# Performance work log

Hardware: AMD Instinct MI355X
Metric: run time of the kernel (lower is better)

The kernel has to match this reference:

```python
import jax, jax.numpy as jnp
import numpy as np

COEF = 0.09          # amount of pixels flipped (salt + pepper)
SALT_VS_PEPPER = 0.5  # skimage default: half salt, half pepper


def setup_inputs() -> dict:
    key = jax.random.key(0)
    images = jax.random.uniform(key, (64, 3, 512, 512), dtype=jnp.float32)
    return {"images": images}


def reference(images):
    # Faithful to skimage.util.random_noise(image, mode='s&p', amount=COEF):
    #   flipped ~ U(0,1) <= amount selects corrupted pixels
    #   salted  ~ U(0,1) <= salt_vs_pepper splits them into salt (1.0) vs pepper (0.0)
    key = jax.random.key(42)
    k_flip, k_salt = jax.random.split(key)
    u_flip = jax.random.uniform(k_flip, images.shape, dtype=images.dtype)
    u_salt = jax.random.uniform(k_salt, images.shape, dtype=images.dtype)
    flipped = u_flip <= COEF
    salted = u_salt <= SALT_VS_PEPPER
    out = jnp.where(flipped & salted, jnp.asarray(1.0, images.dtype), images)
    out = jnp.where(flipped & ~salted, jnp.asarray(0.0, images.dtype), out)
    return out
```

## Files before the change

kernel.cpp:

```cpp
#include <hip/hip_runtime.h>
#include <stdint.h>


__host__ __device__ constexpr uint32_t rotl32(uint32_t x, int r) {
    return (x << r) | (x >> (32 - r));
}

struct TF2 { uint32_t a, b; };

__host__ __device__ constexpr TF2 threefry2x32(uint32_t k0, uint32_t k1,
                                               uint32_t x0, uint32_t x1) {
    const uint32_t ks0 = k0;
    const uint32_t ks1 = k1;
    const uint32_t ks2 = k0 ^ k1 ^ 0x1BD11BDAu;
    x0 += ks0; x1 += ks1;
    x0 += x1; x1 = rotl32(x1, 13); x1 ^= x0;
    x0 += x1; x1 = rotl32(x1, 15); x1 ^= x0;
    x0 += x1; x1 = rotl32(x1, 26); x1 ^= x0;
    x0 += x1; x1 = rotl32(x1,  6); x1 ^= x0;
    x0 += ks1; x1 += ks2 + 1u;
    x0 += x1; x1 = rotl32(x1, 17); x1 ^= x0;
    x0 += x1; x1 = rotl32(x1, 29); x1 ^= x0;
    x0 += x1; x1 = rotl32(x1, 16); x1 ^= x0;
    x0 += x1; x1 = rotl32(x1, 24); x1 ^= x0;
    x0 += ks2; x1 += ks0 + 2u;
    x0 += x1; x1 = rotl32(x1, 13); x1 ^= x0;
    x0 += x1; x1 = rotl32(x1, 15); x1 ^= x0;
    x0 += x1; x1 = rotl32(x1, 26); x1 ^= x0;
    x0 += x1; x1 = rotl32(x1,  6); x1 ^= x0;
    x0 += ks0; x1 += ks1 + 3u;
    x0 += x1; x1 = rotl32(x1, 17); x1 ^= x0;
    x0 += x1; x1 = rotl32(x1, 29); x1 ^= x0;
    x0 += x1; x1 = rotl32(x1, 16); x1 ^= x0;
    x0 += x1; x1 = rotl32(x1, 24); x1 ^= x0;
    x0 += ks1; x1 += ks2 + 4u;
    x0 += x1; x1 = rotl32(x1, 13); x1 ^= x0;
    x0 += x1; x1 = rotl32(x1, 15); x1 ^= x0;
    x0 += x1; x1 = rotl32(x1, 26); x1 ^= x0;
    x0 += x1; x1 = rotl32(x1,  6); x1 ^= x0;
    x0 += ks2; x1 += ks0 + 5u;
    return {x0, x1};
}

constexpr uint32_t SEED_HI = 0u;
constexpr uint32_t SEED_LO = 42u;
constexpr TF2 KFLIP = threefry2x32(SEED_HI, SEED_LO, 0u, 0u);
constexpr TF2 KSALT = threefry2x32(SEED_HI, SEED_LO, 0u, 1u);

constexpr uint32_t FLIP_T = (((uint32_t)((double)0.09f * 8388608.0)) + 1u) << 9;
constexpr uint32_t SALT_T = 0x80000200u;

__device__ __forceinline__ uint32_t rotl_d(uint32_t x, int r) {
    return __builtin_amdgcn_alignbit(x, x, 32u - (uint32_t)r);
}

#define TFR(rot) { x0 += x1; x1 = rotl_d(x1, rot); x1 ^= x0; }

template <uint32_t K0, uint32_t K1>
__device__ __forceinline__ uint32_t tf_bits(uint32_t ctr) {
    constexpr uint32_t K2 = K0 ^ K1 ^ 0x1BD11BDAu;
    uint32_t x0 = K0;
    uint32_t x1 = ctr + K1;
    TFR(13) TFR(15) TFR(26) TFR(6)
    x0 += K1; x1 += K2 + 1u;
    TFR(17) TFR(29) TFR(16) TFR(24)
    x0 += K2; x1 += K0 + 2u;
    TFR(13) TFR(15) TFR(26) TFR(6)
    x0 += K0; x1 += K1 + 3u;
    TFR(17) TFR(29) TFR(16) TFR(24)
    x0 += K1; x1 += K2 + 4u;
    TFR(13) TFR(15) TFR(26) TFR(6)
    x0 += K2; x1 += K0 + 5u;
    return x0 ^ x1;
}

__global__ __launch_bounds__(256)
void ImpulseNoise_32040456028513_kernel(const float4* __restrict__ in,
                                        float4* __restrict__ out,
                                        unsigned n4) {
    unsigned tid = blockIdx.x * blockDim.x + threadIdx.x;
    if (tid >= n4) return;

    float4 v = in[tid];
    float r[4] = {v.x, v.y, v.z, v.w};
    const uint32_t base = tid << 2;

#pragma unroll
    for (int j = 0; j < 4; ++j) {
        const uint32_t i = base + (uint32_t)j;
        uint32_t bits_f = tf_bits<KFLIP.a, KFLIP.b>(i);
        uint32_t bits_s = tf_bits<KSALT.a, KSALT.b>(i);
        float sp = (bits_s < SALT_T) ? 1.0f : 0.0f;
        r[j] = (bits_f < FLIP_T) ? sp : r[j];
    }

    out[tid] = make_float4(r[0], r[1], r[2], r[3]);
}

extern "C" void kernel_launch(void* const* d_in, const int* in_sizes, int n_in,
                              void* d_out, int out_size, void* d_ws, size_t ws_size,
                              hipStream_t stream) {
    const float4* in = (const float4*)d_in[0];
    float4* out = (float4*)d_out;
    unsigned n = (unsigned)in_sizes[0];
    unsigned n4 = n >> 2;
    unsigned blocks = (n4 + 255u) / 256u;
    ImpulseNoise_32040456028513_kernel<<<blocks, 256, 0, stream>>>(in, out, n4);
}
```

Before: 402.4 us.

## Compact flipped pixels per wavefront and compute salt hash only for them

Each wavefront ballots which of its pixels are flipped, compacts their indices into LDS using mbcnt prefix ranks, and then computes the salt Threefry hash only for those compacted indices, 64 at a time. A second ballot redistributes the salt bits back to the owning lanes. Since only about 9% of pixels flip, this is meant to remove most of the second hash computation in a compute-bound kernel. The cost is LDS traffic, extra ballot and popcount work, and a short loop per wave. Skipping the salt hash is exact because the salt value is unused for pixels that are not flipped.

```diff
diff --git a/kernel.cpp b/kernel.cpp
--- a/kernel.cpp
+++ b/kernel.cpp
@@ -74,27 +74,73 @@
     return x0 ^ x1;
 }
 
+__device__ __forceinline__ uint32_t mbcnt64(uint64_t m) {
+    return __builtin_amdgcn_mbcnt_hi((uint32_t)(m >> 32),
+           __builtin_amdgcn_mbcnt_lo((uint32_t)m, 0u));
+}
+
 __global__ __launch_bounds__(256)
 void ImpulseNoise_32040456028513_kernel(const float4* __restrict__ in,
                                         float4* __restrict__ out,
                                         unsigned n4) {
-    unsigned tid = blockIdx.x * blockDim.x + threadIdx.x;
-    if (tid >= n4) return;
+    __shared__ uint32_t slots[1024];
+    const unsigned t = blockIdx.x * 256u + threadIdx.x;
+    if (t >= n4) return;
 
-    float4 v = in[tid];
-    float r[4] = {v.x, v.y, v.z, v.w};
-    const uint32_t base = tid << 2;
+    const unsigned lane = threadIdx.x & 63u;
+    uint32_t* ws = &slots[(threadIdx.x >> 6) << 8];
 
-#pragma unroll
-    for (int j = 0; j < 4; ++j) {
-        const uint32_t i = base + (uint32_t)j;
-        uint32_t bits_f = tf_bits<KFLIP.a, KFLIP.b>(i);
-        uint32_t bits_s = tf_bits<KSALT.a, KSALT.b>(i);
-        float sp = (bits_s < SALT_T) ? 1.0f : 0.0f;
-        r[j] = (bits_f < FLIP_T) ? sp : r[j];
+    const float4 v = in[t];
+    const uint32_t base = t << 2;
+
+    const uint32_t f0 = tf_bits<KFLIP.a, KFLIP.b>(base);
+    const uint32_t f1 = tf_bits<KFLIP.a, KFLIP.b>(base + 1u);
+    const uint32_t f2 = tf_bits<KFLIP.a, KFLIP.b>(base + 2u);
+    const uint32_t f3 = tf_bits<KFLIP.a, KFLIP.b>(base + 3u);
+    const bool flip0 = f0 < FLIP_T;
+    const bool flip1 = f1 < FLIP_T;
+    const bool flip2 = f2 < FLIP_T;
+    const bool flip3 = f3 < FLIP_T;
+
+    const uint64_t B0 = __ballot(flip0);
+    const uint64_t B1 = __ballot(flip1);
+    const uint64_t B2 = __ballot(flip2);
+    const uint64_t B3 = __ballot(flip3);
+
+    const uint32_t cum1 = (uint32_t)__popcll(B0);
+    const uint32_t cum2 = cum1 + (uint32_t)__popcll(B1);
+    const uint32_t cum3 = cum2 + (uint32_t)__popcll(B2);
+    const uint32_t total = cum3 + (uint32_t)__popcll(B3);
+
+    const uint32_t r0 = mbcnt64(B0);
+    const uint32_t r1 = cum1 + mbcnt64(B1);
+    const uint32_t r2 = cum2 + mbcnt64(B2);
+    const uint32_t r3 = cum3 + mbcnt64(B3);
+
+    if (flip0) ws[r0] = base;
+    if (flip1) ws[r1] = base + 1u;
+    if (flip2) ws[r2] = base + 2u;
+    if (flip3) ws[r3] = base + 3u;
+    __threadfence_block();
+
+    uint32_t s0 = 0u, s1 = 0u, s2 = 0u, s3 = 0u;
+    for (uint32_t b = 0; b < total; b += 64u) {
+        const uint32_t ctr = ws[b + lane];
+        const uint32_t h = tf_bits<KSALT.a, KSALT.b>(ctr);
+        const uint64_t S = __ballot(h < SALT_T);
+        const uint32_t d0 = r0 - b, d1 = r1 - b, d2 = r2 - b, d3 = r3 - b;
+        if (d0 < 64u) s0 = (uint32_t)(S >> d0) & 1u;
+        if (d1 < 64u) s1 = (uint32_t)(S >> d1) & 1u;
+        if (d2 < 64u) s2 = (uint32_t)(S >> d2) & 1u;
+        if (d3 < 64u) s3 = (uint32_t)(S >> d3) & 1u;
     }
 
-    out[tid] = make_float4(r[0], r[1], r[2], r[3]);
+    float4 o;
+    o.x = flip0 ? (float)s0 : v.x;
+    o.y = flip1 ? (float)s1 : v.y;
+    o.z = flip2 ? (float)s2 : v.z;
+    o.w = flip3 ? (float)s3 : v.w;
+    out[t] = o;
 }
 
 extern "C" void kernel_launch(void* const* d_in, const int* in_sizes, int n_in,
```

Result: faster. 349.3 us (-13.2%).

## Compute salt hash only for flipped pixels via wave-level stream compaction

Applied to the files above, without the earlier changes.

Each thread now handles eight elements and computes only the flip hash for all of them. Flipped element indices are packed into per-wave shared memory using ballot/mbcnt, and the whole wave then computes the salt Threefry hash only for those packed entries, about 9% of elements. This roughly halves the hash arithmetic, at the cost of LDS traffic, ballots, and the fact that exact element counts must be divisible by eight per thread.

```diff
diff --git a/kernel.cpp b/kernel.cpp
--- a/kernel.cpp
+++ b/kernel.cpp
@@ -74,27 +74,71 @@
     return x0 ^ x1;
 }
 
+__device__ __forceinline__ uint32_t mbcnt64(uint64_t m) {
+    return __builtin_amdgcn_mbcnt_hi((uint32_t)(m >> 32),
+           __builtin_amdgcn_mbcnt_lo((uint32_t)m, 0u));
+}
+
 __global__ __launch_bounds__(256)
 void ImpulseNoise_32040456028513_kernel(const float4* __restrict__ in,
                                         float4* __restrict__ out,
-                                        unsigned n4) {
-    unsigned tid = blockIdx.x * blockDim.x + threadIdx.x;
-    if (tid >= n4) return;
+                                        unsigned nthreads) {
+    __shared__ uint32_t slots[4][512];
+    const unsigned t = blockIdx.x * 256u + threadIdx.x;
+    if (t >= nthreads) return;
 
-    float4 v = in[tid];
-    float r[4] = {v.x, v.y, v.z, v.w};
-    const uint32_t base = tid << 2;
+    const unsigned lane = threadIdx.x & 63u;
+    uint32_t* ws = slots[threadIdx.x >> 6];
 
+    const unsigned w = t >> 6;
+    const unsigned i0 = (w << 7) + lane;
+    const unsigned i1 = i0 + 64u;
+    const float4 va = in[i0];
+    const float4 vb = in[i1];
+    const uint32_t cb0 = i0 << 2;
+    const uint32_t cb1 = i1 << 2;
+
+    uint32_t f[8];
 #pragma unroll
-    for (int j = 0; j < 4; ++j) {
-        const uint32_t i = base + (uint32_t)j;
-        uint32_t bits_f = tf_bits<KFLIP.a, KFLIP.b>(i);
-        uint32_t bits_s = tf_bits<KSALT.a, KSALT.b>(i);
-        float sp = (bits_s < SALT_T) ? 1.0f : 0.0f;
-        r[j] = (bits_f < FLIP_T) ? sp : r[j];
+    for (int j = 0; j < 4; ++j) f[j]     = tf_bits<KFLIP.a, KFLIP.b>(cb0 + (uint32_t)j);
+#pragma unroll
+    for (int j = 0; j < 4; ++j) f[4 + j] = tf_bits<KFLIP.a, KFLIP.b>(cb1 + (uint32_t)j);
+
+    bool flip[8];
+    uint32_t r[8];
+    uint32_t cum = 0u;
+#pragma unroll
+    for (int k = 0; k < 8; ++k) {
+        flip[k] = f[k] < FLIP_T;
+        const uint64_t B = __ballot(flip[k]);
+        r[k] = cum + mbcnt64(B);
+        cum += (uint32_t)__popcll(B);
+        if (flip[k]) ws[r[k]] = ((k < 4) ? cb0 : cb1) + (uint32_t)(k & 3);
     }
+    __threadfence_block();
 
-    out[tid] = make_float4(r[0], r[1], r[2], r[3]);
+    for (uint32_t b = 0; b < cum; b += 64u) {
+        const uint32_t ctr = ws[b + lane];
+        const uint32_t h = tf_bits<KSALT.a, KSALT.b>(ctr);
+        ws[b + lane] = (h < SALT_T) ? 0x3F800000u : 0u;
+    }
+    __threadfence_block();
+
+    float s[8];
+#pragma unroll
+    for (int k = 0; k < 8; ++k) s[k] = __uint_as_float(ws[r[k]]);
+
+    float4 oa, ob;
+    oa.x = flip[0] ? s[0] : va.x;
+    oa.y = flip[1] ? s[1] : va.y;
+    oa.z = flip[2] ? s[2] : va.z;
+    oa.w = flip[3] ? s[3] : va.w;
+    ob.x = flip[4] ? s[4] : vb.x;
+    ob.y = flip[5] ? s[5] : vb.y;
+    ob.z = flip[6] ? s[6] : vb.z;
+    ob.w = flip[7] ? s[7] : vb.w;
+    out[i0] = oa;
+    out[i1] = ob;
 }
 
 extern "C" void kernel_launch(void* const* d_in, const int* in_sizes, int n_in,
@@ -103,7 +147,7 @@
     const float4* in = (const float4*)d_in[0];
     float4* out = (float4*)d_out;
     unsigned n = (unsigned)in_sizes[0];
-    unsigned n4 = n >> 2;
-    unsigned blocks = (n4 + 255u) / 256u;
-    ImpulseNoise_32040456028513_kernel<<<blocks, 256, 0, stream>>>(in, out, n4);
+    unsigned nthreads = n >> 3;
+    unsigned blocks = (nthreads + 255u) / 256u;
+    ImpulseNoise_32040456028513_kernel<<<blocks, 256, 0, stream>>>(in, out, nthreads);
 }
```

New measurement: 332.6 us. 1.21x faster.
